# Performance work log

Measured on AMD Instinct MI355X. Metric: run time of the kernel, lower is better.

## Reference

```python
import jax, jax.numpy as jnp
import numpy as np

D_MODEL = 1024
NUM_HEADS = 16
HEAD_DIM = D_MODEL // NUM_HEADS  # 64
THETA = 10000.0
B, S = 2, 2048


def setup_inputs() -> dict:
    key = jax.random.key(0)
    k1, k2, k3 = jax.random.split(key, 3)
    sigma_qkv = (2.0 / (D_MODEL + 3 * D_MODEL)) ** 0.5
    sigma_o = (2.0 / (D_MODEL + D_MODEL)) ** 0.5
    x = jax.random.normal(k1, (B, S, D_MODEL), dtype=jnp.float32)
    w_qkv = jax.random.normal(k2, (3 * D_MODEL, D_MODEL), dtype=jnp.float32) * sigma_qkv
    w_o = jax.random.normal(k3, (D_MODEL, D_MODEL), dtype=jnp.float32) * sigma_o
    token_positions = jnp.arange(S, dtype=jnp.int32)
    return {"x": x, "w_qkv": w_qkv, "w_o": w_o, "token_positions": token_positions, "mask": 1}


def _rope(t, pos):
    # t: (B, H, S, HEAD_DIM); pos: (S,) int
    ids = jnp.arange(HEAD_DIM // 2, dtype=jnp.float32)
    freqs = pos.astype(jnp.float32)[:, None] * (THETA ** (-2.0 * ids / HEAD_DIM))  # (S, HEAD_DIM/2)
    cos, sin = jnp.cos(freqs), jnp.sin(freqs)
    even, odd = t[..., 0::2], t[..., 1::2]
    r_even = even * cos - odd * sin
    r_odd = odd * cos + even * sin
    # interleave back to original layout
    return jnp.stack([r_even, r_odd], axis=-1).reshape(t.shape)


def reference(x, w_qkv, w_o, token_positions, mask):
    # fused QKV projection: Linear computes x @ W^T with W [out, in]
    qkv = x @ w_qkv.T  # (B, S, 3*D_MODEL)
    q, k, v = jnp.split(qkv, 3, axis=-1)

    def to_heads(t):
        return t.reshape(B, S, NUM_HEADS, HEAD_DIM).transpose(0, 2, 1, 3)  # (B, H, S, Dh)

    q, k, v = to_heads(q), to_heads(k), to_heads(v)
    q = _rope(q, token_positions)
    k = _rope(k, token_positions)

    scores = jnp.einsum('bhqd,bhkd->bhqk', q, k)
    if mask:  # causal: lower-triangular allowed
        causal = jnp.tril(jnp.ones((S, S), dtype=bool))
        scores = jnp.where(causal, scores, -jnp.inf)
    attn = jax.nn.softmax(scores * (HEAD_DIM ** -0.5), axis=-1)
    out = jnp.einsum('bhqk,bhkd->bhqd', attn, v)  # (B, H, S, Dh)
    out = out.transpose(0, 2, 1, 3).reshape(B, S, D_MODEL)
    return out @ w_o.T
```

## Files before the change

### kernel.cpp

```cpp
#include <hip/hip_runtime.h>
#include <hip/hip_bf16.h>
#include <math.h>

typedef __bf16 bf16_t;
typedef __bf16 bf16x8 __attribute__((ext_vector_type(8)));
typedef __bf16 bf16x4 __attribute__((ext_vector_type(4)));
typedef float  f32x4  __attribute__((ext_vector_type(4)));

#define D_MODEL 1024
#define NH      16
#define HD      64
#define BATCH   2
#define SEQ     2048
#define MROWS   (BATCH*SEQ)
#define QKVN    (3*D_MODEL)
#define FA_PAD  72
#define SCALE_LOG2E 0.18033688011112042f

__device__ __forceinline__ void async_cp16(const bf16_t* g, bf16_t* l) {
    __builtin_amdgcn_global_load_lds(
        (const __attribute__((address_space(1))) void*)g,
        (__attribute__((address_space(3))) void*)l,
        16, 0, 0);
}

__global__ void cvt_all(const float* __restrict__ x, const float* __restrict__ wq,
                        const float* __restrict__ wo,
                        bf16_t* __restrict__ xb, bf16_t* __restrict__ wqb,
                        bf16_t* __restrict__ wob) {
    const int nx = MROWS * D_MODEL, nq = QKVN * D_MODEL;
    int i = (blockIdx.x * blockDim.x + threadIdx.x) * 4;
    const float* s; bf16_t* d; int off;
    if (i < nx)           { s = x;  d = xb;  off = i; }
    else if (i < nx + nq) { s = wq; d = wqb; off = i - nx; }
    else                  { s = wo; d = wob; off = i - nx - nq; }
    float4 v = *(const float4*)(s + off);
    d[off]     = (bf16_t)v.x;
    d[off + 1] = (bf16_t)v.y;
    d[off + 2] = (bf16_t)v.z;
    d[off + 3] = (bf16_t)v.w;
}

template <typename OutT, int NI>
__global__ __launch_bounds__(256) void gemm_nt(const bf16_t* __restrict__ A,
                                               const bf16_t* __restrict__ Bm,
                                               OutT* __restrict__ C,
                                               int M, int N, int K) {
    __shared__ __align__(16) bf16_t As[128 * 32];
    __shared__ __align__(16) bf16_t Bs[NI * 32 * 32];
    const int tid  = threadIdx.x;
    const int w    = tid >> 6;
    const int lane = tid & 63;
    const int quad = lane >> 4;
    const int l16  = lane & 15;
    const int m0   = blockIdx.x * 128;
    const int n0   = blockIdx.y * (NI * 32);
    const int wm   = (w >> 1) * 64;
    const int wn   = (w & 1) * (NI * 16);

    f32x4 acc[4][NI];
    #pragma unroll
    for (int i = 0; i < 4; i++)
        #pragma unroll
        for (int j = 0; j < NI; j++)
            acc[i][j] = (f32x4){0.f, 0.f, 0.f, 0.f};

    const bf16_t* Ag0 = A  + (size_t)(m0 + (tid >> 2)) * K + (tid & 3) * 8;
    const bf16_t* Ag1 = Ag0 + (size_t)64 * K;
    const bf16_t* Bg0 = Bm + (size_t)(n0 + (tid >> 2)) * K + (tid & 3) * 8;
    const bf16_t* Bg1 = Bg0 + (size_t)64 * K;
    bf16_t* Al0 = &As[(size_t)tid * 8];
    bf16_t* Al1 = &As[((size_t)tid + 256) * 8];
    bf16_t* Bl0 = &Bs[(size_t)tid * 8];
    bf16_t* Bl1 = &Bs[((size_t)tid + 256) * 8];

    for (int k0 = 0; k0 < K; k0 += 32) {
        async_cp16(Ag0 + k0, Al0);
        async_cp16(Ag1 + k0, Al1);
        async_cp16(Bg0 + k0, Bl0);
        if (NI == 4) async_cp16(Bg1 + k0, Bl1);
        __syncthreads();

        bf16x8 af[4], bfr[NI];
        #pragma unroll
        for (int mi = 0; mi < 4; mi++)
            af[mi] = *(const bf16x8*)&As[(wm + mi * 16 + l16) * 32 + quad * 8];
        #pragma unroll
        for (int ni = 0; ni < NI; ni++)
            bfr[ni] = *(const bf16x8*)&Bs[(wn + ni * 16 + l16) * 32 + quad * 8];
        #pragma unroll
        for (int mi = 0; mi < 4; mi++)
            #pragma unroll
            for (int ni = 0; ni < NI; ni++)
                acc[mi][ni] = __builtin_amdgcn_mfma_f32_16x16x32_bf16(
                    af[mi], bfr[ni], acc[mi][ni], 0, 0, 0);
        __syncthreads();
    }

    #pragma unroll
    for (int mi = 0; mi < 4; mi++)
        #pragma unroll
        for (int ni = 0; ni < NI; ni++) {
            const int col = n0 + wn + ni * 16 + l16;
            #pragma unroll
            for (int r = 0; r < 4; r++) {
                const int row = m0 + wm + mi * 16 + quad * 4 + r;
                C[(size_t)row * N + col] = (OutT)acc[mi][ni][r];
            }
        }
}

__global__ __launch_bounds__(256) void rope_split(const bf16_t* __restrict__ qkv,
                                                  const int* __restrict__ pos,
                                                  bf16_t* __restrict__ Qh,
                                                  bf16_t* __restrict__ Kh,
                                                  bf16_t* __restrict__ VT) {
    __shared__ bf16_t vs[128][FA_PAD];
    const int tid   = threadIdx.x;
    const int s_loc = tid >> 1;
    const int half  = tid & 1;
    const int s0    = blockIdx.x * 128;
    const int bh    = blockIdx.y;
    const int b     = bh >> 4, h = bh & 15;
    const int s     = s0 + s_loc;

    const bf16_t* row = qkv + (size_t)(b * SEQ + s) * QKVN + h * HD + half * 32;

    bf16_t qbuf[32], kbuf[32], vbuf[32];
    #pragma unroll
    for (int j = 0; j < 4; j++) {
        *(bf16x8*)&qbuf[j * 8] = *(const bf16x8*)(row + j * 8);
        *(bf16x8*)&kbuf[j * 8] = *(const bf16x8*)(row + D_MODEL + j * 8);
        *(bf16x8*)&vbuf[j * 8] = *(const bf16x8*)(row + 2 * D_MODEL + j * 8);
    }

    const float pf = (float)pos[s];
    #pragma unroll
    for (int p = 0; p < 16; p++) {
        const int d2 = half * 16 + p;
        const float inv = __expf(-0.28782313662425575f * (float)d2);
        const float f = pf * inv;
        const float c = cosf(f), sn = sinf(f);
        float qe = (float)qbuf[2 * p], qo = (float)qbuf[2 * p + 1];
        float ke = (float)kbuf[2 * p], ko = (float)kbuf[2 * p + 1];
        qbuf[2 * p]     = (bf16_t)(qe * c - qo * sn);
        qbuf[2 * p + 1] = (bf16_t)(qo * c + qe * sn);
        kbuf[2 * p]     = (bf16_t)(ke * c - ko * sn);
        kbuf[2 * p + 1] = (bf16_t)(ko * c + ke * sn);
    }

    bf16_t* qdst = Qh + ((size_t)bh * SEQ + s) * HD + half * 32;
    bf16_t* kdst = Kh + ((size_t)bh * SEQ + s) * HD + half * 32;
    #pragma unroll
    for (int j = 0; j < 4; j++) {
        *(bf16x8*)(qdst + j * 8) = *(bf16x8*)&qbuf[j * 8];
        *(bf16x8*)(kdst + j * 8) = *(bf16x8*)&kbuf[j * 8];
        *(bf16x8*)&vs[s_loc][half * 32 + j * 8] = *(bf16x8*)&vbuf[j * 8];
    }
    __syncthreads();

    const int d  = tid >> 2;
    const int sc = tid & 3;
    bf16_t tmp[32];
    #pragma unroll
    for (int i = 0; i < 32; i++) tmp[i] = vs[sc * 32 + i][d];
    bf16_t* vdst = VT + ((size_t)bh * HD + d) * SEQ + s0 + sc * 32;
    #pragma unroll
    for (int j = 0; j < 4; j++)
        *(bf16x8*)(vdst + j * 8) = *(bf16x8*)&tmp[j * 8];
}

__global__ __launch_bounds__(256) void flash_attn(const bf16_t* __restrict__ Qh,
                                                  const bf16_t* __restrict__ Kh,
                                                  const bf16_t* __restrict__ VT,
                                                  bf16_t* __restrict__ AO) {
    __shared__ __align__(16) bf16_t Ks[64 * FA_PAD];
    __shared__ __align__(16) bf16_t Vs[64 * FA_PAD];
    __shared__ __align__(16) bf16_t pT[4][16][FA_PAD];

    const int tid  = threadIdx.x;
    const int w    = tid >> 6;
    const int lane = tid & 63;
    const int quad = lane >> 4;
    const int l16  = lane & 15;

    const int bid  = blockIdx.x;
    const int bh   = bid & 31;
    const int tb   = bid >> 5;
    const int u    = tb & 7;
    const int qtr  = tb >> 3;
    const int my_t = (qtr == 0) ? (31 - u)
                   : (qtr == 1) ? (16 + u)
                   : (qtr == 2) ? (15 - u) : u;
    const int nkv  = my_t + 1;

    const bf16_t* Qb = Qh + (size_t)bh * SEQ * HD;
    const bf16_t* Kb = Kh + (size_t)bh * SEQ * HD;
    const bf16_t* Vb = VT + (size_t)bh * HD * SEQ;

    const int q0 = my_t * 64 + w * 16;
    const bf16x8 aq0 = *(const bf16x8*)(Qb + (size_t)(q0 + l16) * HD + quad * 8);
    const bf16x8 aq1 = *(const bf16x8*)(Qb + (size_t)(q0 + l16) * HD + 32 + quad * 8);

    const int srow = tid >> 3, scol = (tid & 7) * 8;
    const int lds0 = srow * FA_PAD + scol;
    const int lds1 = (srow + 32) * FA_PAD + scol;

    f32x4 o[4];
    #pragma unroll
    for (int i = 0; i < 4; i++) o[i] = (f32x4){0.f, 0.f, 0.f, 0.f};
    float lsum = 0.f;

    bf16x8 pK0 = *(const bf16x8*)(Kb + (size_t)srow * HD + scol);
    bf16x8 pK1 = *(const bf16x8*)(Kb + (size_t)(srow + 32) * HD + scol);
    bf16x8 pV0 = *(const bf16x8*)(Vb + (size_t)srow * SEQ + scol);
    bf16x8 pV1 = *(const bf16x8*)(Vb + (size_t)(srow + 32) * SEQ + scol);

    for (int kt = 0; kt < nkv; ++kt) {
        *(bf16x8*)&Ks[lds0] = pK0;
        *(bf16x8*)&Ks[lds1] = pK1;
        *(bf16x8*)&Vs[lds0] = pV0;
        *(bf16x8*)&Vs[lds1] = pV1;
        __syncthreads();

        if (kt + 1 < nkv) {
            const int kn = (kt + 1) * 64;
            pK0 = *(const bf16x8*)(Kb + (size_t)(kn + srow) * HD + scol);
            pK1 = *(const bf16x8*)(Kb + (size_t)(kn + srow + 32) * HD + scol);
            pV0 = *(const bf16x8*)(Vb + (size_t)srow * SEQ + kn + scol);
            pV1 = *(const bf16x8*)(Vb + (size_t)(srow + 32) * SEQ + kn + scol);
        }

        const bool diag = (kt == my_t);

        #pragma unroll
        for (int ni = 0; ni < 4; ni++) {
            if (diag && ni > w) {
                *(bf16x4*)&pT[w][l16][ni * 16 + quad * 4] = (bf16x4){0, 0, 0, 0};
                continue;
            }
            bf16x8 kb0 = *(const bf16x8*)&Ks[(ni * 16 + l16) * FA_PAD + quad * 8];
            bf16x8 kb1 = *(const bf16x8*)&Ks[(ni * 16 + l16) * FA_PAD + 32 + quad * 8];
            f32x4 t = (f32x4){0.f, 0.f, 0.f, 0.f};
            t = __builtin_amdgcn_mfma_f32_16x16x32_bf16(kb0, aq0, t, 0, 0, 0);
            t = __builtin_amdgcn_mfma_f32_16x16x32_bf16(kb1, aq1, t, 0, 0, 0);
            bf16x4 pk;
            #pragma unroll
            for (int r = 0; r < 4; r++) {
                float pv = exp2f(t[r] * SCALE_LOG2E);
                if (diag && (ni * 16 + quad * 4 + r > w * 16 + l16)) pv = 0.f;
                lsum += pv;
                pk[r] = (bf16_t)pv;
            }
            *(bf16x4*)&pT[w][l16][ni * 16 + quad * 4] = pk;
        }

        #pragma unroll
        for (int ks = 0; ks < 2; ks++) {
            if (diag && w * 16 + 15 < ks * 32) continue;
            bf16x8 ap = *(const bf16x8*)&pT[w][l16][ks * 32 + quad * 8];
            #pragma unroll
            for (int ni = 0; ni < 4; ni++) {
                bf16x8 vb = *(const bf16x8*)&Vs[(ni * 16 + l16) * FA_PAD + ks * 32 + quad * 8];
                o[ni] = __builtin_amdgcn_mfma_f32_16x16x32_bf16(ap, vb, o[ni], 0, 0, 0);
            }
        }

        __syncthreads();
    }

    lsum += __shfl_xor(lsum, 16);
    lsum += __shfl_xor(lsum, 32);
    f32x4 linv;
    #pragma unroll
    for (int r = 0; r < 4; r++)
        linv[r] = 1.0f / __shfl(lsum, quad * 4 + r);

    const int b = bh >> 4, hh = bh & 15;
    #pragma unroll
    for (int ni = 0; ni < 4; ni++) {
        #pragma unroll
        for (int r = 0; r < 4; r++) {
            const size_t row = (size_t)b * SEQ + q0 + quad * 4 + r;
            AO[row * D_MODEL + hh * HD + ni * 16 + l16] = (bf16_t)(o[ni][r] * linv[r]);
        }
    }
}

extern "C" void kernel_launch(void* const* d_in, const int* in_sizes, int n_in,
                              void* d_out, int out_size, void* d_ws, size_t ws_size,
                              hipStream_t stream) {
    const float* x     = (const float*)d_in[0];
    const float* w_qkv = (const float*)d_in[1];
    const float* w_o   = (const float*)d_in[2];
    const int*   tpos  = (const int*)d_in[3];
    float*       out   = (float*)d_out;

    char* ws = (char*)d_ws;
    bf16_t* xb  = (bf16_t*)(ws);
    bf16_t* wqb = (bf16_t*)(ws + 8388608);
    bf16_t* wob = (bf16_t*)(ws + 14680064);
    bf16_t* qkv = (bf16_t*)(ws + 16777216);
    bf16_t* Qh  = (bf16_t*)(ws + 41943040);
    bf16_t* Kh  = (bf16_t*)(ws + 50331648);
    bf16_t* VT  = (bf16_t*)(ws + 58720256);
    bf16_t* AO  = (bf16_t*)(ws + 67108864);

    cvt_all<<<8192, 256, 0, stream>>>(x, w_qkv, w_o, xb, wqb, wob);

    gemm_nt<bf16_t, 4><<<dim3(32, 24), 256, 0, stream>>>(xb, wqb, qkv, MROWS, QKVN, D_MODEL);

    rope_split<<<dim3(SEQ / 128, BATCH * NH), 256, 0, stream>>>(qkv, tpos, Qh, Kh, VT);

    flash_attn<<<1024, 256, 0, stream>>>(Qh, Kh, VT, AO);

    gemm_nt<float, 2><<<dim3(32, 16), 256, 0, stream>>>(AO, wob, out, MROWS, D_MODEL, D_MODEL);
}
```

Measured before the change: 195.2 us.

## Split KV range across warps in flash attention with LDS merge of partial outputs

The attention kernel now has each warp cover all 64 query rows of the tile and take its own 32-key slice of every 128-key chunk. K and V fragments are read straight from global memory into registers with a two-deep software prefetch, so the shared K/V staging and its per-tile barriers are gone. Each warp's partial output and row sums are then summed through shared memory at the end. Block scheduling is simplified to a descending tile order, and launch bounds now request two blocks per CU. The cost is many more registers per thread, a large shared-memory merge buffer, and uncoalesced V reads from global.

```diff
diff --git a/kernel.cpp b/kernel.cpp
--- a/kernel.cpp
+++ b/kernel.cpp
@@ -15,6 +15,7 @@
 #define MROWS   (BATCH*SEQ)
 #define QKVN    (3*D_MODEL)
 #define FA_PAD  72
+#define PADK    40
 #define SCALE_LOG2E 0.18033688011112042f
 
 __device__ __forceinline__ void async_cp16(const bf16_t* g, bf16_t* l) {
@@ -170,13 +171,11 @@
         *(bf16x8*)(vdst + j * 8) = *(bf16x8*)&tmp[j * 8];
 }
 
-__global__ __launch_bounds__(256) void flash_attn(const bf16_t* __restrict__ Qh,
-                                                  const bf16_t* __restrict__ Kh,
-                                                  const bf16_t* __restrict__ VT,
-                                                  bf16_t* __restrict__ AO) {
-    __shared__ __align__(16) bf16_t Ks[64 * FA_PAD];
-    __shared__ __align__(16) bf16_t Vs[64 * FA_PAD];
-    __shared__ __align__(16) bf16_t pT[4][16][FA_PAD];
+__global__ __launch_bounds__(256, 2) void flash_attn(const bf16_t* __restrict__ Qh,
+                                                     const bf16_t* __restrict__ Kh,
+                                                     const bf16_t* __restrict__ VT,
+                                                     bf16_t* __restrict__ AO) {
+    __shared__ __align__(16) float mrg[4 * 64 * 66 + 256];
 
     const int tid  = threadIdx.x;
     const int w    = tid >> 6;
@@ -186,105 +185,132 @@
 
     const int bid  = blockIdx.x;
     const int bh   = bid & 31;
-    const int tb   = bid >> 5;
-    const int u    = tb & 7;
-    const int qtr  = tb >> 3;
-    const int my_t = (qtr == 0) ? (31 - u)
-                   : (qtr == 1) ? (16 + u)
-                   : (qtr == 2) ? (15 - u) : u;
-    const int nkv  = my_t + 1;
+    const int my_t = 31 - (bid >> 5);
+    const int q0   = my_t * 64;
+    const int qmax = q0 + 63;
+    const int nch  = (my_t + 2) >> 1;
 
     const bf16_t* Qb = Qh + (size_t)bh * SEQ * HD;
     const bf16_t* Kb = Kh + (size_t)bh * SEQ * HD;
     const bf16_t* Vb = VT + (size_t)bh * HD * SEQ;
 
-    const int q0 = my_t * 64 + w * 16;
-    const bf16x8 aq0 = *(const bf16x8*)(Qb + (size_t)(q0 + l16) * HD + quad * 8);
-    const bf16x8 aq1 = *(const bf16x8*)(Qb + (size_t)(q0 + l16) * HD + 32 + quad * 8);
-
-    const int srow = tid >> 3, scol = (tid & 7) * 8;
-    const int lds0 = srow * FA_PAD + scol;
-    const int lds1 = (srow + 32) * FA_PAD + scol;
-
-    f32x4 o[4];
-    #pragma unroll
-    for (int i = 0; i < 4; i++) o[i] = (f32x4){0.f, 0.f, 0.f, 0.f};
-    float lsum = 0.f;
-
-    bf16x8 pK0 = *(const bf16x8*)(Kb + (size_t)srow * HD + scol);
-    bf16x8 pK1 = *(const bf16x8*)(Kb + (size_t)(srow + 32) * HD + scol);
-    bf16x8 pV0 = *(const bf16x8*)(Vb + (size_t)srow * SEQ + scol);
-    bf16x8 pV1 = *(const bf16x8*)(Vb + (size_t)(srow + 32) * SEQ + scol);
-
-    for (int kt = 0; kt < nkv; ++kt) {
-        *(bf16x8*)&Ks[lds0] = pK0;
-        *(bf16x8*)&Ks[lds1] = pK1;
-        *(bf16x8*)&Vs[lds0] = pV0;
-        *(bf16x8*)&Vs[lds1] = pV1;
-        __syncthreads();
-
-        if (kt + 1 < nkv) {
-            const int kn = (kt + 1) * 64;
-            pK0 = *(const bf16x8*)(Kb + (size_t)(kn + srow) * HD + scol);
-            pK1 = *(const bf16x8*)(Kb + (size_t)(kn + srow + 32) * HD + scol);
-            pV0 = *(const bf16x8*)(Vb + (size_t)srow * SEQ + kn + scol);
-            pV1 = *(const bf16x8*)(Vb + (size_t)(srow + 32) * SEQ + kn + scol);
-        }
-
-        const bool diag = (kt == my_t);
-
-        #pragma unroll
-        for (int ni = 0; ni < 4; ni++) {
-            if (diag && ni > w) {
-                *(bf16x4*)&pT[w][l16][ni * 16 + quad * 4] = (bf16x4){0, 0, 0, 0};
-                continue;
+    bf16_t* pTw = (bf16_t*)mrg + w * (64 * PADK);
+
+    bf16x8 aq[4][2];
+    #pragma unroll
+    for (int qi = 0; qi < 4; qi++) {
+        aq[qi][0] = *(const bf16x8*)(Qb + (size_t)(q0 + qi * 16 + l16) * HD + quad * 8);
+        aq[qi][1] = *(const bf16x8*)(Qb + (size_t)(q0 + qi * 16 + l16) * HD + 32 + quad * 8);
+    }
+
+    f32x4 o[4][4];
+    #pragma unroll
+    for (int qi = 0; qi < 4; qi++)
+        #pragma unroll
+        for (int di = 0; di < 4; di++)
+            o[qi][di] = (f32x4){0.f, 0.f, 0.f, 0.f};
+    float ls[4] = {0.f, 0.f, 0.f, 0.f};
+
+#define LOADK(KB, CC) do {                                                     \
+    const int _cl = (CC) < nch ? (CC) : nch - 1;                               \
+    const bf16_t* _kp = Kb + (size_t)(_cl * 128 + w * 32 + l16) * HD + quad * 8; \
+    KB[0][0] = *(const bf16x8*)_kp;                                            \
+    KB[0][1] = *(const bf16x8*)(_kp + 32);                                     \
+    KB[1][0] = *(const bf16x8*)(_kp + 16 * HD);                                \
+    KB[1][1] = *(const bf16x8*)(_kp + 16 * HD + 32);                           \
+} while (0)
+
+#define FA_STEP(KB, CC) do {                                                   \
+    const int _kvb = (CC) * 128 + w * 32;                                      \
+    if (_kvb <= qmax) {                                                        \
+        bf16x8 vf[4];                                                          \
+        _Pragma("unroll")                                                      \
+        for (int di = 0; di < 4; di++)                                         \
+            vf[di] = *(const bf16x8*)(Vb + (size_t)(di * 16 + l16) * SEQ + _kvb + quad * 8); \
+        const bool _full = (_kvb + 31 <= q0);                                  \
+        _Pragma("unroll")                                                      \
+        for (int qi = 0; qi < 4; qi++) {                                       \
+            _Pragma("unroll")                                                  \
+            for (int mi = 0; mi < 2; mi++) {                                   \
+                if (!_full && _kvb + mi * 16 > qmax) {                         \
+                    *(bf16x4*)&pTw[(qi * 16 + l16) * PADK + mi * 16 + quad * 4] = (bf16x4){0, 0, 0, 0}; \
+                    continue;                                                  \
+                }                                                              \
+                f32x4 t = (f32x4){0.f, 0.f, 0.f, 0.f};                         \
+                t = __builtin_amdgcn_mfma_f32_16x16x32_bf16(KB[0 + mi][0], aq[qi][0], t, 0, 0, 0); \
+                t = __builtin_amdgcn_mfma_f32_16x16x32_bf16(KB[0 + mi][1], aq[qi][1], t, 0, 0, 0); \
+                bf16x4 pk;                                                     \
+                _Pragma("unroll")                                              \
+                for (int r = 0; r < 4; r++) {                                  \
+                    float pv = exp2f(t[r] * SCALE_LOG2E);                      \
+                    if (!_full && (_kvb + mi * 16 + quad * 4 + r > q0 + qi * 16 + l16)) pv = 0.f; \
+                    ls[qi] += pv;                                              \
+                    pk[r] = (bf16_t)pv;                                        \
+                }                                                              \
+                *(bf16x4*)&pTw[(qi * 16 + l16) * PADK + mi * 16 + quad * 4] = pk; \
+            }                                                                  \
+        }                                                                      \
+        _Pragma("unroll")                                                      \
+        for (int qi = 0; qi < 4; qi++) {                                       \
+            bf16x8 ap = *(const bf16x8*)&pTw[(qi * 16 + l16) * PADK + quad * 8]; \
+            _Pragma("unroll")                                                  \
+            for (int di = 0; di < 4; di++)                                     \
+                o[qi][di] = __builtin_amdgcn_mfma_f32_16x16x32_bf16(ap, vf[di], o[qi][di], 0, 0, 0); \
+        }                                                                      \
+    }                                                                          \
+} while (0)
+
+    bf16x8 kA[2][2], kB2[2][2];
+    LOADK(kA, 0);
+    for (int c2 = 0; c2 < nch; c2 += 2) {
+        LOADK(kB2, c2 + 1);
+        FA_STEP(kA, c2);
+        if (c2 + 1 < nch) {
+            LOADK(kA, c2 + 2);
+            FA_STEP(kB2, c2 + 1);
+        }
+    }
+
+    __syncthreads();
+    {
+        float* mw = mrg + w * 4224;
+        #pragma unroll
+        for (int qi = 0; qi < 4; qi++) {
+            #pragma unroll
+            for (int di = 0; di < 4; di++)
+                #pragma unroll
+                for (int r = 0; r < 4; r++)
+                    mw[(qi * 16 + quad * 4 + r) * 66 + di * 16 + l16] = o[qi][di][r];
+            ls[qi] += __shfl_xor(ls[qi], 16);
+            ls[qi] += __shfl_xor(ls[qi], 32);
+        }
+        float* lsp = mrg + 4 * 4224;
+        if (quad == 0) {
+            #pragma unroll
+            for (int qi = 0; qi < 4; qi++)
+                lsp[w * 64 + qi * 16 + l16] = ls[qi];
+        }
+    }
+    __syncthreads();
+    {
+        const float* lsp = mrg + 4 * 4224;
+        const int b = bh >> 4, hh = bh & 15;
+        #pragma unroll
+        for (int r = 0; r < 4; r++) {
+            const int q = w * 16 + quad * 4 + r;
+            const float lr = lsp[q] + lsp[64 + q] + lsp[128 + q] + lsp[192 + q];
+            const float li = 1.0f / lr;
+            #pragma unroll
+            for (int di = 0; di < 4; di++) {
+                const int d = di * 16 + l16;
+                const float v = mrg[q * 66 + d] + mrg[4224 + q * 66 + d]
+                              + mrg[8448 + q * 66 + d] + mrg[12672 + q * 66 + d];
+                AO[((size_t)b * SEQ + q0 + q) * D_MODEL + hh * HD + d] = (bf16_t)(v * li);
             }
-            bf16x8 kb0 = *(const bf16x8*)&Ks[(ni * 16 + l16) * FA_PAD + quad * 8];
-            bf16x8 kb1 = *(const bf16x8*)&Ks[(ni * 16 + l16) * FA_PAD + 32 + quad * 8];
-            f32x4 t = (f32x4){0.f, 0.f, 0.f, 0.f};
-            t = __builtin_amdgcn_mfma_f32_16x16x32_bf16(kb0, aq0, t, 0, 0, 0);
-            t = __builtin_amdgcn_mfma_f32_16x16x32_bf16(kb1, aq1, t, 0, 0, 0);
-            bf16x4 pk;
-            #pragma unroll
-            for (int r = 0; r < 4; r++) {
-                float pv = exp2f(t[r] * SCALE_LOG2E);
-                if (diag && (ni * 16 + quad * 4 + r > w * 16 + l16)) pv = 0.f;
-                lsum += pv;
-                pk[r] = (bf16_t)pv;
-            }
-            *(bf16x4*)&pT[w][l16][ni * 16 + quad * 4] = pk;
-        }
-
-        #pragma unroll
-        for (int ks = 0; ks < 2; ks++) {
-            if (diag && w * 16 + 15 < ks * 32) continue;
-            bf16x8 ap = *(const bf16x8*)&pT[w][l16][ks * 32 + quad * 8];
-            #pragma unroll
-            for (int ni = 0; ni < 4; ni++) {
-                bf16x8 vb = *(const bf16x8*)&Vs[(ni * 16 + l16) * FA_PAD + ks * 32 + quad * 8];
-                o[ni] = __builtin_amdgcn_mfma_f32_16x16x32_bf16(ap, vb, o[ni], 0, 0, 0);
-            }
-        }
-
-        __syncthreads();
-    }
-
-    lsum += __shfl_xor(lsum, 16);
-    lsum += __shfl_xor(lsum, 32);
-    f32x4 linv;
-    #pragma unroll
-    for (int r = 0; r < 4; r++)
-        linv[r] = 1.0f / __shfl(lsum, quad * 4 + r);
-
-    const int b = bh >> 4, hh = bh & 15;
-    #pragma unroll
-    for (int ni = 0; ni < 4; ni++) {
-        #pragma unroll
-        for (int r = 0; r < 4; r++) {
-            const size_t row = (size_t)b * SEQ + q0 + quad * 4 + r;
-            AO[row * D_MODEL + hh * HD + ni * 16 + l16] = (bf16_t)(o[ni][r] * linv[r]);
-        }
-    }
+        }
+    }
+#undef LOADK
+#undef FA_STEP
 }
 
 extern "C" void kernel_launch(void* const* d_in, const int* in_sizes, int n_in,
```

Measured after the change: 201.4 us. 3.1% more time.

## Use 32x32 MFMA tiles with split-KV warps and shared-memory merge in flash attention

Applied to the files above, without the earlier changes.

Restructures the attention kernel so each wave computes a 32x32 query-by-key block with 32x32x16 MFMA instructions. The four waves split into two query halves and two key halves, and the key-half partial outputs and row sums are combined through shared memory at the end. It also drops the interleaved tile-to-block scheduling in favour of a simple descending order, and uses a raw v_exp_f32 in place of exp2f. The intent is fewer MFMA issues and less LDS fragment traffic per tile, at the cost of an extra merge step, more registers and possibly worse load balance.

```diff
diff --git a/kernel.cpp b/kernel.cpp
--- a/kernel.cpp
+++ b/kernel.cpp
@@ -6,6 +6,7 @@
 typedef __bf16 bf16x8 __attribute__((ext_vector_type(8)));
 typedef __bf16 bf16x4 __attribute__((ext_vector_type(4)));
 typedef float  f32x4  __attribute__((ext_vector_type(4)));
+typedef float  f32x16 __attribute__((ext_vector_type(16)));
 
 #define D_MODEL 1024
 #define NH      16
@@ -15,6 +16,7 @@
 #define MROWS   (BATCH*SEQ)
 #define QKVN    (3*D_MODEL)
 #define FA_PAD  72
+#define PADK    40
 #define SCALE_LOG2E 0.18033688011112042f
 
 __device__ __forceinline__ void async_cp16(const bf16_t* g, bf16_t* l) {
@@ -22,6 +24,12 @@
         (const __attribute__((address_space(1))) void*)g,
         (__attribute__((address_space(3))) void*)l,
         16, 0, 0);
+}
+
+__device__ __forceinline__ float fexp2(float x) {
+    float r;
+    asm("v_exp_f32 %0, %1" : "=v"(r) : "v"(x));
+    return r;
 }
 
 __global__ void cvt_all(const float* __restrict__ x, const float* __restrict__ wq,
@@ -174,47 +182,54 @@
                                                   const bf16_t* __restrict__ Kh,
                                                   const bf16_t* __restrict__ VT,
                                                   bf16_t* __restrict__ AO) {
-    __shared__ __align__(16) bf16_t Ks[64 * FA_PAD];
-    __shared__ __align__(16) bf16_t Vs[64 * FA_PAD];
-    __shared__ __align__(16) bf16_t pT[4][16][FA_PAD];
+    __shared__ __align__(16) char smem[64 * FA_PAD * 2 * 2 + 4 * 32 * PADK * 2];
+    bf16_t* Ks = (bf16_t*)smem;
+    bf16_t* Vs = Ks + 64 * FA_PAD;
+    bf16_t* pT = Vs + 64 * FA_PAD;
 
     const int tid  = threadIdx.x;
     const int w    = tid >> 6;
     const int lane = tid & 63;
-    const int quad = lane >> 4;
-    const int l16  = lane & 15;
+    const int l31  = lane & 31;
+    const int hi   = lane >> 5;
+    const int qh   = w & 1;
+    const int kh   = w >> 1;
 
     const int bid  = blockIdx.x;
     const int bh   = bid & 31;
-    const int tb   = bid >> 5;
-    const int u    = tb & 7;
-    const int qtr  = tb >> 3;
-    const int my_t = (qtr == 0) ? (31 - u)
-                   : (qtr == 1) ? (16 + u)
-                   : (qtr == 2) ? (15 - u) : u;
+    const int my_t = 31 - (bid >> 5);
     const int nkv  = my_t + 1;
 
     const bf16_t* Qb = Qh + (size_t)bh * SEQ * HD;
     const bf16_t* Kb = Kh + (size_t)bh * SEQ * HD;
     const bf16_t* Vb = VT + (size_t)bh * HD * SEQ;
 
-    const int q0 = my_t * 64 + w * 16;
-    const bf16x8 aq0 = *(const bf16x8*)(Qb + (size_t)(q0 + l16) * HD + quad * 8);
-    const bf16x8 aq1 = *(const bf16x8*)(Qb + (size_t)(q0 + l16) * HD + 32 + quad * 8);
+    const int q0b = my_t * 64;
+    const int qlo = q0b + qh * 32;
+    const int qg  = qlo + l31;
+
+    bf16x8 aq[4];
+    #pragma unroll
+    for (int ks = 0; ks < 4; ks++)
+        aq[ks] = *(const bf16x8*)(Qb + (size_t)qg * HD + ks * 16 + hi * 8);
 
     const int srow = tid >> 3, scol = (tid & 7) * 8;
     const int lds0 = srow * FA_PAD + scol;
     const int lds1 = (srow + 32) * FA_PAD + scol;
 
-    f32x4 o[4];
-    #pragma unroll
-    for (int i = 0; i < 4; i++) o[i] = (f32x4){0.f, 0.f, 0.f, 0.f};
-    float lsum = 0.f;
+    f32x16 o[2];
+    #pragma unroll
+    for (int dt = 0; dt < 2; dt++)
+        #pragma unroll
+        for (int i = 0; i < 16; i++) o[dt][i] = 0.f;
+    float ls = 0.f;
 
     bf16x8 pK0 = *(const bf16x8*)(Kb + (size_t)srow * HD + scol);
     bf16x8 pK1 = *(const bf16x8*)(Kb + (size_t)(srow + 32) * HD + scol);
     bf16x8 pV0 = *(const bf16x8*)(Vb + (size_t)srow * SEQ + scol);
     bf16x8 pV1 = *(const bf16x8*)(Vb + (size_t)(srow + 32) * SEQ + scol);
+
+    bf16_t* pb = &pT[(w * 32 + l31) * PADK];
 
     for (int kt = 0; kt < nkv; ++kt) {
         *(bf16x8*)&Ks[lds0] = pK0;
@@ -231,58 +246,78 @@
             pV1 = *(const bf16x8*)(Vb + (size_t)(srow + 32) * SEQ + kn + scol);
         }
 
-        const bool diag = (kt == my_t);
-
-        #pragma unroll
-        for (int ni = 0; ni < 4; ni++) {
-            if (diag && ni > w) {
-                *(bf16x4*)&pT[w][l16][ni * 16 + quad * 4] = (bf16x4){0, 0, 0, 0};
-                continue;
+        const int kvbw = kt * 64 + kh * 32;
+        if (kvbw <= qlo + 31) {
+            const bool full = (kvbw + 31 <= qlo);
+
+            bf16x8 kb[4];
+            #pragma unroll
+            for (int ks = 0; ks < 4; ks++)
+                kb[ks] = *(const bf16x8*)&Ks[(kh * 32 + l31) * FA_PAD + ks * 16 + hi * 8];
+            f32x16 t;
+            #pragma unroll
+            for (int i = 0; i < 16; i++) t[i] = 0.f;
+            #pragma unroll
+            for (int ks = 0; ks < 4; ks++)
+                t = __builtin_amdgcn_mfma_f32_32x32x16_bf16(kb[ks], aq[ks], t, 0, 0, 0);
+
+            bf16x4 pk[4];
+            #pragma unroll
+            for (int r = 0; r < 16; r++) {
+                float pv = fexp2(t[r] * SCALE_LOG2E);
+                if (!full) {
+                    const int kvg = kvbw + (r & 3) + 8 * (r >> 2) + 4 * hi;
+                    if (kvg > qg) pv = 0.f;
+                }
+                ls += pv;
+                pk[r >> 2][r & 3] = (bf16_t)pv;
             }
-            bf16x8 kb0 = *(const bf16x8*)&Ks[(ni * 16 + l16) * FA_PAD + quad * 8];
-            bf16x8 kb1 = *(const bf16x8*)&Ks[(ni * 16 + l16) * FA_PAD + 32 + quad * 8];
-            f32x4 t = (f32x4){0.f, 0.f, 0.f, 0.f};
-            t = __builtin_amdgcn_mfma_f32_16x16x32_bf16(kb0, aq0, t, 0, 0, 0);
-            t = __builtin_amdgcn_mfma_f32_16x16x32_bf16(kb1, aq1, t, 0, 0, 0);
-            bf16x4 pk;
-            #pragma unroll
-            for (int r = 0; r < 4; r++) {
-                float pv = exp2f(t[r] * SCALE_LOG2E);
-                if (diag && (ni * 16 + quad * 4 + r > w * 16 + l16)) pv = 0.f;
-                lsum += pv;
-                pk[r] = (bf16_t)pv;
+            #pragma unroll
+            for (int g = 0; g < 4; g++)
+                *(bf16x4*)&pb[8 * g + 4 * hi] = pk[g];
+
+            bf16x8 pa0 = *(const bf16x8*)&pb[hi * 8];
+            bf16x8 pa1 = *(const bf16x8*)&pb[16 + hi * 8];
+            #pragma unroll
+            for (int dt = 0; dt < 2; dt++) {
+                const int vbase = (dt * 32 + l31) * FA_PAD + kh * 32 + hi * 8;
+                bf16x8 vf0 = *(const bf16x8*)&Vs[vbase];
+                bf16x8 vf1 = *(const bf16x8*)&Vs[vbase + 16];
+                o[dt] = __builtin_amdgcn_mfma_f32_32x32x16_bf16(pa0, vf0, o[dt], 0, 0, 0);
+                o[dt] = __builtin_amdgcn_mfma_f32_32x32x16_bf16(pa1, vf1, o[dt], 0, 0, 0);
             }
-            *(bf16x4*)&pT[w][l16][ni * 16 + quad * 4] = pk;
-        }
-
-        #pragma unroll
-        for (int ks = 0; ks < 2; ks++) {
-            if (diag && w * 16 + 15 < ks * 32) continue;
-            bf16x8 ap = *(const bf16x8*)&pT[w][l16][ks * 32 + quad * 8];
-            #pragma unroll
-            for (int ni = 0; ni < 4; ni++) {
-                bf16x8 vb = *(const bf16x8*)&Vs[(ni * 16 + l16) * FA_PAD + ks * 32 + quad * 8];
-                o[ni] = __builtin_amdgcn_mfma_f32_16x16x32_bf16(ap, vb, o[ni], 0, 0, 0);
+        }
+
+        __syncthreads();
+    }
+
+    ls += __shfl_xor(ls, 32);
+    float* mrgO = (float*)smem;
+    float* lsp  = mrgO + 2 * 32 * 66;
+    if (kh == 1) {
+        #pragma unroll
+        for (int r = 0; r < 16; r++) {
+            const int qlc = (r & 3) + 8 * (r >> 2) + 4 * hi;
+            #pragma unroll
+            for (int dt = 0; dt < 2; dt++)
+                mrgO[(qh * 32 + qlc) * 66 + dt * 32 + l31] = o[dt][r];
+        }
+        if (hi == 0) lsp[qh * 32 + l31] = ls;
+    }
+    __syncthreads();
+    if (kh == 0) {
+        const float lt = ls + lsp[qh * 32 + l31];
+        const int b = bh >> 4, hh = bh & 15;
+        #pragma unroll
+        for (int r = 0; r < 16; r++) {
+            const int qlc = (r & 3) + 8 * (r >> 2) + 4 * hi;
+            const float li = 1.0f / __shfl(lt, qlc);
+            const size_t row = (size_t)b * SEQ + q0b + qh * 32 + qlc;
+            #pragma unroll
+            for (int dt = 0; dt < 2; dt++) {
+                const float v = o[dt][r] + mrgO[(qh * 32 + qlc) * 66 + dt * 32 + l31];
+                AO[row * D_MODEL + hh * HD + dt * 32 + l31] = (bf16_t)(v * li);
             }
-        }
-
-        __syncthreads();
-    }
-
-    lsum += __shfl_xor(lsum, 16);
-    lsum += __shfl_xor(lsum, 32);
-    f32x4 linv;
-    #pragma unroll
-    for (int r = 0; r < 4; r++)
-        linv[r] = 1.0f / __shfl(lsum, quad * 4 + r);
-
-    const int b = bh >> 4, hh = bh & 15;
-    #pragma unroll
-    for (int ni = 0; ni < 4; ni++) {
-        #pragma unroll
-        for (int r = 0; r < 4; r++) {
-            const size_t row = (size_t)b * SEQ + q0 + quad * 4 + r;
-            AO[row * D_MODEL + hh * HD + ni * 16 + l16] = (bf16_t)(o[ni][r] * linv[r]);
         }
     }
 }
```

Result: no change. 193.8 us (-0.7%).
